# Optimization experiments

Measured on AMD Instinct MI355X. Metric: run time of the kernel, lower is better.

## Reference

```python
import jax, jax.numpy as jnp
import numpy as np

N_NODES = 100000
N_EDGES = 3200000
IN_CH, HID, OUT_CH = 128, 16, 64


def gcn_conv(x, W, b, row, col, n_nodes):
    # PyG GCNConv: add self loops, symmetric deg^{-1/2} normalization,
    # linear transform, scatter-add aggregation at target nodes (col).
    x = x @ W  # [N, out]
    deg = jax.ops.segment_sum(jnp.ones_like(col, dtype=x.dtype), col,
                              num_segments=n_nodes)  # includes self loops
    inv_sqrt = jnp.where(deg > 0, jax.lax.rsqrt(deg), 0.0)
    norm = inv_sqrt[row] * inv_sqrt[col]  # [E+N]
    msgs = x[row] * norm[:, None]  # gather + scale
    out = jax.ops.segment_sum(msgs, col, num_segments=n_nodes)
    return out + b


def setup_inputs() -> dict:
    key = jax.random.key(0)
    ks = jax.random.split(key, 12)
    x = jax.random.normal(ks[0], (N_NODES, IN_CH), dtype=jnp.float32)
    edge_index = jax.random.randint(ks[1], (2, N_EDGES), 0, N_NODES, dtype=jnp.int64)

    def glorot(k, fan_in, fan_out):
        s = jnp.sqrt(6.0 / (fan_in + fan_out))
        return jax.random.uniform(k, (fan_in, fan_out), jnp.float32, -s, s)

    return {
        'x': x,
        'edge_index': edge_index,
        'conv1_W': glorot(ks[2], IN_CH, HID),
        'conv1_b': jnp.zeros((HID,), jnp.float32),
        'conv2_W': glorot(ks[3], HID, OUT_CH),
        'conv2_b': jnp.zeros((OUT_CH,), jnp.float32),
        't1_W': glorot(ks[4], IN_CH, HID),
        't1_b': jnp.zeros((HID,), jnp.float32),
        't2_W': glorot(ks[5], HID, OUT_CH),
        't2_b': jnp.zeros((OUT_CH,), jnp.float32),
    }


def reference(x, edge_index, conv1_W, conv1_b, conv2_W, conv2_b,
              t1_W, t1_b, t2_W, t2_b):
    n = x.shape[0]
    # add self loops once (fixed shape)
    loops = jnp.arange(n, dtype=edge_index.dtype)
    row = jnp.concatenate([edge_index[0], loops])
    col = jnp.concatenate([edge_index[1], loops])

    identity1 = x @ t1_W + t1_b
    h = jax.nn.relu(gcn_conv(x, conv1_W, conv1_b, row, col, n)) + identity1
    identity2 = h @ t2_W + t2_b
    out = jax.nn.relu(gcn_conv(h, conv2_W, conv2_b, row, col, n)) + identity2
    return out
```

## Files before the change

### kernel.cpp

```cpp
#include <hip/hip_runtime.h>

#define INCH 128
#define C1   16
#define C2   64
#define LOCB 7
#define BNODES (1 << LOCB)
#define CAP  8192
#define ROWBITS 17
#define ROWMASK ((1 << ROWBITS) - 1)
#define SENT 0xFFFFFFFFu
#define ACC2P 9
#define FXS   16384.0f
#define INVFX 6.103515625e-05f
#define FXBH  524288.5f
#define BSH   19
#define BKT_T 1024
#define AGG_T 512

typedef int iv4 __attribute__((ext_vector_type(4)));
typedef unsigned long long ulv2 __attribute__((ext_vector_type(2)));

__global__ void binit_kernel(int* __restrict__ gcur, int K) {
    int t = blockIdx.x * blockDim.x + threadIdx.x;
    if (t < K) gcur[t] = t * CAP;
}

__global__ __launch_bounds__(BKT_T) void bucket_kernel(
    const int* __restrict__ row, const int* __restrict__ col,
    int* __restrict__ gcur, int* __restrict__ barr,
    int e, int n, int K, int nblocks)
{
    __shared__ int cnt[1024];
    __shared__ int cur[1024];
    __shared__ int sst[1024];
    int tid = threadIdx.x;
    int e4 = e >> 2;
    long b0 = (long)blockIdx.x * e4 / nblocks;
    long b1 = (long)(blockIdx.x + 1) * e4 / nblocks;
    const iv4* c4p = (const iv4*)col;
    const iv4* r4p = (const iv4*)row;
    cnt[tid] = 0;
    __syncthreads();
    for (long i = b0 + tid; i < b1; i += BKT_T) {
        iv4 c4 = c4p[i], r4 = r4p[i];
        #pragma unroll
        for (int k = 0; k < 4; ++k) {
            unsigned c = (unsigned)c4[k], r = (unsigned)r4[k];
            if (c < (unsigned)n && r < (unsigned)n)
                atomicAdd(&cnt[c >> LOCB], 1);
        }
    }
    if (blockIdx.x == 0) {
        for (int i = e4 * 4 + tid; i < e; i += BKT_T) {
            unsigned c = (unsigned)col[i], r = (unsigned)row[i];
            if (c < (unsigned)n && r < (unsigned)n)
                atomicAdd(&cnt[c >> LOCB], 1);
        }
    }
    __syncthreads();
    if (tid < K) {
        int c = cnt[tid];
        int start = c ? atomicAdd(&gcur[tid], (c + 15) & ~15) : 0;
        cur[tid] = start;
        sst[tid] = start;
    }
    __syncthreads();
    for (long i = b0 + tid; i < b1; i += BKT_T) {
        iv4 c4 = c4p[i], r4 = r4p[i];
        #pragma unroll
        for (int k = 0; k < 4; ++k) {
            unsigned c = (unsigned)c4[k], r = (unsigned)r4[k];
            if (c < (unsigned)n && r < (unsigned)n) {
                int b = c >> LOCB;
                int slot = atomicAdd(&cur[b], 1);
                if ((unsigned)slot < (unsigned)((b + 1) * CAP))
                    barr[slot] = (int)(r | ((c & (BNODES - 1)) << ROWBITS));
            }
        }
    }
    if (blockIdx.x == 0) {
        for (int i = e4 * 4 + tid; i < e; i += BKT_T) {
            unsigned c = (unsigned)col[i], r = (unsigned)row[i];
            if (c < (unsigned)n && r < (unsigned)n) {
                int b = c >> LOCB;
                int slot = atomicAdd(&cur[b], 1);
                if ((unsigned)slot < (unsigned)((b + 1) * CAP))
                    barr[slot] = (int)(r | ((c & (BNODES - 1)) << ROWBITS));
            }
        }
    }
    __syncthreads();
    if (tid < K) {
        int c = cnt[tid];
        if (c) {
            int start = sst[tid];
            int end = start + c;
            int re  = start + ((c + 15) & ~15);
            int lim = (tid + 1) * CAP;
            if (end > lim) end = lim;
            if (re  > lim) re  = lim;
            for (int j = end; j < re; ++j) barr[j] = (int)SENT;
        }
    }
}

__global__ __launch_bounds__(AGG_T) void degree_kernel(
    const int* __restrict__ barr, const int* __restrict__ gcur,
    int* __restrict__ deg, int n)
{
    __shared__ int lcnt[BNODES];
    int b = blockIdx.x, tid = threadIdx.x;
    if (tid < BNODES) lcnt[tid] = 0;
    __syncthreads();
    int base = b * CAP;
    int len = gcur[b] - base;
    if (len < 0) len = 0;
    if (len > CAP) len = CAP;
    int len4 = len >> 2;
    const iv4* b4 = (const iv4*)(barr + base);
    for (int i = tid; i < len4; i += AGG_T) {
        iv4 p4 = b4[i];
        #pragma unroll
        for (int k = 0; k < 4; ++k) {
            unsigned pk = (unsigned)p4[k];
            if ((pk & ROWMASK) < (unsigned)n)
                atomicAdd(&lcnt[(pk >> ROWBITS) & (BNODES - 1)], 1);
        }
    }
    __syncthreads();
    if (tid < BNODES) {
        int node = (b << LOCB) + tid;
        if (node < n) deg[node] = lcnt[tid];
    }
}

__global__ __launch_bounds__(256) void linear1_kernel(
    const float* __restrict__ x, const float* __restrict__ W1,
    const float* __restrict__ T1, const float* __restrict__ t1b,
    const int* __restrict__ deg,
    unsigned* __restrict__ xW1u, float* __restrict__ xT1, int n)
{
    __shared__ float Wc[INCH][32];
    __shared__ float xs[16][INCH + 4];
    int tid = threadIdx.x;

    for (int i = tid; i < INCH * C1; i += 256) {
        int k = i / C1, c = i % C1;
        Wc[k][c]      = W1[i];
        Wc[k][c + 16] = T1[i];
    }
    int node0 = blockIdx.x * 16;
    for (int i = tid; i < 16 * (INCH / 4); i += 256) {
        int r = i / (INCH / 4);
        int cc = i % (INCH / 4);
        int node = node0 + r;
        float4 v = make_float4(0.f, 0.f, 0.f, 0.f);
        if (node < n) v = ((const float4*)x)[(size_t)node * (INCH / 4) + cc];
        ((float4*)&xs[r][0])[cc] = v;
    }
    __syncthreads();

    int ch = tid & 15, nl = tid >> 4;
    int node = node0 + nl;
    if (node >= n) return;
    float a1 = 0.f, a2 = 0.f;
    #pragma unroll
    for (int k = 0; k < INCH; ++k) {
        float xv = xs[nl][k];
        a1 += xv * Wc[k][ch];
        a2 += xv * Wc[k][ch + 16];
    }
    float ic = rsqrtf((float)(deg[node] + 1));
    xW1u[(node << 4) + ch] = (unsigned)(a1 * ic * FXS + FXBH);
    xT1[(node << 4) + ch]  = a2 + t1b[ch];
}

#define EDGE_GS(PK, GA, GB)                                                   \
    do {                                                                      \
        if (((PK) & ROWMASK) < un) {                                          \
            unsigned long long* _a = &acc[(((PK) >> ROWBITS) & (BNODES - 1))][tb]; \
            atomicAdd(&_a[0], (GA)[0]);                                       \
            atomicAdd(&_a[1], (GA)[1]);                                       \
            atomicAdd(&_a[2], (GB)[0]);                                       \
            atomicAdd(&_a[3], (GB)[1]);                                       \
        }                                                                     \
    } while (0)

#define GATHER_SCATTER(SRCBUF)                                                \
    {                                                                         \
        int jj = tid >> 1;                                                    \
        for (int i0 = jj * 4; i0 + 3 < len; i0 += (AGG_T * 2)) {              \
            iv4 w = *(const iv4*)(bp + i0);                                   \
            unsigned s0 = (unsigned)w[0] & ROWMASK, s1 = (unsigned)w[1] & ROWMASK; \
            unsigned s2 = (unsigned)w[2] & ROWMASK, s3 = (unsigned)w[3] & ROWMASK; \
            unsigned c0 = s0 < un ? s0 : 0u, c1 = s1 < un ? s1 : 0u;          \
            unsigned c2 = s2 < un ? s2 : 0u, c3 = s3 < un ? s3 : 0u;          \
            const ulv2* p0 = (const ulv2*)(SRCBUF + ((size_t)c0 << 4) + chb); \
            const ulv2* p1 = (const ulv2*)(SRCBUF + ((size_t)c1 << 4) + chb); \
            const ulv2* p2 = (const ulv2*)(SRCBUF + ((size_t)c2 << 4) + chb); \
            const ulv2* p3 = (const ulv2*)(SRCBUF + ((size_t)c3 << 4) + chb); \
            ulv2 ga0 = p0[0], gb0 = p0[1];                                    \
            ulv2 ga1 = p1[0], gb1 = p1[1];                                    \
            ulv2 ga2 = p2[0], gb2 = p2[1];                                    \
            ulv2 ga3 = p3[0], gb3 = p3[1];                                    \
            EDGE_GS((unsigned)w[0], ga0, gb0);                                \
            EDGE_GS((unsigned)w[1], ga1, gb1);                                \
            EDGE_GS((unsigned)w[2], ga2, gb2);                                \
            EDGE_GS((unsigned)w[3], ga3, gb3);                                \
        }                                                                     \
    }

__global__ __launch_bounds__(AGG_T) void agg1_bucket_kernel(
    const int* __restrict__ barr, const int* __restrict__ gcur,
    const int* __restrict__ deg, const unsigned* __restrict__ xW1u,
    const float* __restrict__ xT1, const float* __restrict__ b1,
    float* __restrict__ h, unsigned* __restrict__ hu, int n)
{
    __shared__ unsigned long long acc[BNODES][ACC2P];
    int b = blockIdx.x, tid = threadIdx.x;
    for (int i = tid; i < BNODES * ACC2P; i += AGG_T) (&acc[0][0])[i] = 0ull;
    __syncthreads();

    int base = b * CAP;
    int len = gcur[b] - base;
    if (len < 0) len = 0;
    if (len > CAP) len = CAP;
    const int* bp = barr + base;
    unsigned un = (unsigned)n;
    int chb = (tid & 1) << 3;
    int tb  = (tid & 1) << 2;

    GATHER_SCATTER(xW1u)
    __syncthreads();

    const unsigned* au = (const unsigned*)&acc[0][0];
    for (int t = tid; t < BNODES * C1; t += AGG_T) {
        int loc = t >> 4, ch = t & 15;
        int node = (b << LOCB) + loc;
        if (node >= n) continue;
        int idx = (node << 4) + ch;
        int dg = deg[node];
        unsigned wd = au[loc * (2 * ACC2P) + ch];
        int tot = (int)(wd + xW1u[idx] - ((unsigned)(dg + 1) << BSH));
        float ic = rsqrtf((float)(dg + 1));
        float v = (float)tot * INVFX * ic + b1[ch];
        float hv = fmaxf(v, 0.f) + xT1[idx];
        h[idx]  = hv;
        hu[idx] = (unsigned)(hv * ic * FXS + FXBH);
    }
}

__global__ __launch_bounds__(AGG_T) void agg2_bucket_kernel(
    const int* __restrict__ barr, const int* __restrict__ gcur,
    const int* __restrict__ deg, const unsigned* __restrict__ hu,
    const float* __restrict__ h,
    const float* __restrict__ W2, const float* __restrict__ T2,
    const float* __restrict__ b2, const float* __restrict__ t2b,
    float* __restrict__ out, int n)
{
    __shared__ unsigned long long acc[BNODES][ACC2P];
    __shared__ float Wc[C1][128];
    __shared__ float h_s[BNODES][C1];
    __shared__ float accf[BNODES][C1 + 1];
    int b = blockIdx.x, tid = threadIdx.x;
    for (int i = tid; i < BNODES * ACC2P; i += AGG_T) (&acc[0][0])[i] = 0ull;
    for (int i = tid; i < C1 * 128; i += AGG_T) {
        int k = i >> 7, c = i & 127;
        Wc[k][c] = (c < 64) ? W2[k * C2 + c] : T2[k * C2 + (c - 64)];
    }
    {
        int node0 = b << LOCB;
        for (int t = tid; t < BNODES * C1 / 4; t += AGG_T) {
            float4 v = make_float4(0.f, 0.f, 0.f, 0.f);
            if (node0 + (t >> 2) < n) v = ((const float4*)h)[(size_t)node0 * 4 + t];
            ((float4*)&h_s[0][0])[t] = v;
        }
    }
    __syncthreads();

    int base = b * CAP;
    int len = gcur[b] - base;
    if (len < 0) len = 0;
    if (len > CAP) len = CAP;
    const int* bp = barr + base;
    unsigned un = (unsigned)n;
    int chb = (tid & 1) << 3;
    int tb  = (tid & 1) << 2;

    GATHER_SCATTER(hu)
    __syncthreads();

    const unsigned* au = (const unsigned*)&acc[0][0];
    for (int t = tid; t < BNODES * C1; t += AGG_T) {
        int loc = t >> 4, ch = t & 15;
        int node = (b << LOCB) + loc;
        float v = 0.f;
        if (node < n) {
            int dg = deg[node];
            unsigned wd = au[loc * (2 * ACC2P) + ch];
            int tot = (int)(wd + hu[(node << 4) + ch] - ((unsigned)(dg + 1) << BSH));
            v = (float)tot * INVFX * rsqrtf((float)(dg + 1));
        }
        accf[loc][ch] = v;
    }
    __syncthreads();

    int och = tid & 63, g = tid >> 6;
    float w1r[C1], w2r[C1];
    #pragma unroll
    for (int k = 0; k < C1; ++k) { w1r[k] = Wc[k][och]; w2r[k] = Wc[k][och + 64]; }
    float bb = b2[och], tb2 = t2b[och];
    for (int q = 0; q < 16; ++q) {
        int loc = (g << 4) + q;
        int node2 = (b << LOCB) + loc;
        if (node2 >= n) continue;
        float s1 = bb, s2 = tb2;
        #pragma unroll
        for (int k = 0; k < C1; ++k) {
            s1 += accf[loc][k] * w1r[k];
            s2 += h_s[loc][k]  * w2r[k];
        }
        out[(size_t)node2 * C2 + och] = fmaxf(s1, 0.f) + s2;
    }
}

extern "C" void kernel_launch(void* const* d_in, const int* in_sizes, int n_in,
                              void* d_out, int out_size, void* d_ws, size_t ws_size,
                              hipStream_t stream) {
    const float* x   = (const float*)d_in[0];
    const int*   ei  = (const int*)d_in[1];
    const float* W1  = (const float*)d_in[2];
    const float* b1  = (const float*)d_in[3];
    const float* W2  = (const float*)d_in[4];
    const float* b2  = (const float*)d_in[5];
    const float* T1  = (const float*)d_in[6];
    const float* t1b = (const float*)d_in[7];
    const float* T2  = (const float*)d_in[8];
    const float* t2b = (const float*)d_in[9];
    float* out = (float*)d_out;

    const int n = in_sizes[0] / INCH;
    const int e = in_sizes[1] / 2;
    const int* row = ei;
    const int* col = ei + e;
    const int K = (n + BNODES - 1) >> LOCB;

    char* ws = (char*)d_ws;
    int*      gcur = (int*)ws;                        ws += 4096;
    int*      deg  = (int*)ws;                        ws += (size_t)n * 4;
    float*    xT1  = (float*)ws;                      ws += (size_t)n * C1 * 4;
    float*    h    = (float*)ws;                      ws += (size_t)n * C1 * 4;
    unsigned* xW1u = (unsigned*)ws;                   ws += (size_t)n * C1 * 4;
    unsigned* hu   = (unsigned*)ws;                   ws += (size_t)n * C1 * 4;
    int*      barr = (int*)ws;                        ws += (size_t)K * CAP * 4;

    const int nbb = 390;

    binit_kernel  <<<(K + 255) / 256, 256, 0, stream>>>(gcur, K);
    bucket_kernel <<<nbb, BKT_T, 0, stream>>>(row, col, gcur, barr, e, n, K, nbb);
    degree_kernel <<<K, AGG_T, 0, stream>>>(barr, gcur, deg, n);

    linear1_kernel <<<(n + 15) / 16, 256, 0, stream>>>(x, W1, T1, t1b, deg, xW1u, xT1, n);
    agg1_bucket_kernel<<<K, AGG_T, 0, stream>>>(barr, gcur, deg, xW1u, xT1, b1, h, hu, n);
    agg2_bucket_kernel<<<K, AGG_T, 0, stream>>>(barr, gcur, deg, hu, h,
                                                W2, T2, b2, t2b, out, n);
}
```

Baseline: 268.9 us.

## Compress gathered node features to 16-bit fixed point with clamping

```diff
diff --git a/kernel.cpp b/kernel.cpp
--- a/kernel.cpp
+++ b/kernel.cpp
@@ -10,15 +10,14 @@
 #define ROWMASK ((1 << ROWBITS) - 1)
 #define SENT 0xFFFFFFFFu
 #define ACC2P 9
-#define FXS   16384.0f
-#define INVFX 6.103515625e-05f
-#define FXBH  524288.5f
-#define BSH   19
+#define FXS   512.0f
+#define INVFX 0.001953125f
+#define U16B  32768.5f
+#define BSH   15
 #define BKT_T 1024
 #define AGG_T 512
 
 typedef int iv4 __attribute__((ext_vector_type(4)));
-typedef unsigned long long ulv2 __attribute__((ext_vector_type(2)));
 
 __global__ void binit_kernel(int* __restrict__ gcur, int K) {
     int t = blockIdx.x * blockDim.x + threadIdx.x;
@@ -134,11 +133,16 @@
     }
 }
 
+__device__ __forceinline__ unsigned short enc16(float v) {
+    float c = fminf(fmaxf(v, -63.0f), 63.0f);
+    return (unsigned short)(c * FXS + U16B);
+}
+
 __global__ __launch_bounds__(256) void linear1_kernel(
     const float* __restrict__ x, const float* __restrict__ W1,
     const float* __restrict__ T1, const float* __restrict__ t1b,
     const int* __restrict__ deg,
-    unsigned* __restrict__ xW1u, float* __restrict__ xT1, int n)
+    unsigned short* __restrict__ xu16, float* __restrict__ xT1, int n)
 {
     __shared__ float Wc[INCH][32];
     __shared__ float xs[16][INCH + 4];
@@ -171,22 +175,24 @@
         a2 += xv * Wc[k][ch + 16];
     }
     float ic = rsqrtf((float)(deg[node] + 1));
-    xW1u[(node << 4) + ch] = (unsigned)(a1 * ic * FXS + FXBH);
+    xu16[(node << 4) + ch] = enc16(a1 * ic);
     xT1[(node << 4) + ch]  = a2 + t1b[ch];
 }
 
-#define EDGE_GS(PK, GA, GB)                                                   \
+#define EDGE_GS(PK, G)                                                        \
     do {                                                                      \
         if (((PK) & ROWMASK) < un) {                                          \
             unsigned long long* _a = &acc[(((PK) >> ROWBITS) & (BNODES - 1))][tb]; \
-            atomicAdd(&_a[0], (GA)[0]);                                       \
-            atomicAdd(&_a[1], (GA)[1]);                                       \
-            atomicAdd(&_a[2], (GB)[0]);                                       \
-            atomicAdd(&_a[3], (GB)[1]);                                       \
+            _Pragma("unroll")                                                 \
+            for (int _j = 0; _j < 4; ++_j) {                                  \
+                unsigned _d = (unsigned)(G)[_j];                              \
+                atomicAdd(&_a[_j],                                            \
+                    ((unsigned long long)(_d >> 16) << 32) | (_d & 0xFFFFu)); \
+            }                                                                 \
         }                                                                     \
     } while (0)
 
-#define GATHER_SCATTER(SRCBUF)                                                \
+#define GATHER_SCATTER(TBL)                                                   \
     {                                                                         \
         int jj = tid >> 1;                                                    \
         for (int i0 = jj * 4; i0 + 3 < len; i0 += (AGG_T * 2)) {              \
@@ -195,26 +201,22 @@
             unsigned s2 = (unsigned)w[2] & ROWMASK, s3 = (unsigned)w[3] & ROWMASK; \
             unsigned c0 = s0 < un ? s0 : 0u, c1 = s1 < un ? s1 : 0u;          \
             unsigned c2 = s2 < un ? s2 : 0u, c3 = s3 < un ? s3 : 0u;          \
-            const ulv2* p0 = (const ulv2*)(SRCBUF + ((size_t)c0 << 4) + chb); \
-            const ulv2* p1 = (const ulv2*)(SRCBUF + ((size_t)c1 << 4) + chb); \
-            const ulv2* p2 = (const ulv2*)(SRCBUF + ((size_t)c2 << 4) + chb); \
-            const ulv2* p3 = (const ulv2*)(SRCBUF + ((size_t)c3 << 4) + chb); \
-            ulv2 ga0 = p0[0], gb0 = p0[1];                                    \
-            ulv2 ga1 = p1[0], gb1 = p1[1];                                    \
-            ulv2 ga2 = p2[0], gb2 = p2[1];                                    \
-            ulv2 ga3 = p3[0], gb3 = p3[1];                                    \
-            EDGE_GS((unsigned)w[0], ga0, gb0);                                \
-            EDGE_GS((unsigned)w[1], ga1, gb1);                                \
-            EDGE_GS((unsigned)w[2], ga2, gb2);                                \
-            EDGE_GS((unsigned)w[3], ga3, gb3);                                \
+            iv4 g0 = *(const iv4*)(TBL + ((size_t)c0 << 3) + tb4);            \
+            iv4 g1 = *(const iv4*)(TBL + ((size_t)c1 << 3) + tb4);            \
+            iv4 g2 = *(const iv4*)(TBL + ((size_t)c2 << 3) + tb4);            \
+            iv4 g3 = *(const iv4*)(TBL + ((size_t)c3 << 3) + tb4);            \
+            EDGE_GS((unsigned)w[0], g0);                                      \
+            EDGE_GS((unsigned)w[1], g1);                                      \
+            EDGE_GS((unsigned)w[2], g2);                                      \
+            EDGE_GS((unsigned)w[3], g3);                                      \
         }                                                                     \
     }
 
 __global__ __launch_bounds__(AGG_T) void agg1_bucket_kernel(
     const int* __restrict__ barr, const int* __restrict__ gcur,
-    const int* __restrict__ deg, const unsigned* __restrict__ xW1u,
+    const int* __restrict__ deg, const unsigned short* __restrict__ xu16,
     const float* __restrict__ xT1, const float* __restrict__ b1,
-    float* __restrict__ h, unsigned* __restrict__ hu, int n)
+    float* __restrict__ h, unsigned short* __restrict__ hu16, int n)
 {
     __shared__ unsigned long long acc[BNODES][ACC2P];
     int b = blockIdx.x, tid = threadIdx.x;
@@ -226,11 +228,12 @@
     if (len < 0) len = 0;
     if (len > CAP) len = CAP;
     const int* bp = barr + base;
+    const unsigned* tblw = (const unsigned*)xu16;
     unsigned un = (unsigned)n;
-    int chb = (tid & 1) << 3;
+    int tb4 = (tid & 1) << 2;
     int tb  = (tid & 1) << 2;
 
-    GATHER_SCATTER(xW1u)
+    GATHER_SCATTER(tblw)
     __syncthreads();
 
     const unsigned* au = (const unsigned*)&acc[0][0];
@@ -241,18 +244,18 @@
         int idx = (node << 4) + ch;
         int dg = deg[node];
         unsigned wd = au[loc * (2 * ACC2P) + ch];
-        int tot = (int)(wd + xW1u[idx] - ((unsigned)(dg + 1) << BSH));
+        int tot = (int)(wd + xu16[idx] - ((unsigned)(dg + 1) << BSH));
         float ic = rsqrtf((float)(dg + 1));
         float v = (float)tot * INVFX * ic + b1[ch];
         float hv = fmaxf(v, 0.f) + xT1[idx];
-        h[idx]  = hv;
-        hu[idx] = (unsigned)(hv * ic * FXS + FXBH);
+        h[idx]    = hv;
+        hu16[idx] = enc16(hv * ic);
     }
 }
 
 __global__ __launch_bounds__(AGG_T) void agg2_bucket_kernel(
     const int* __restrict__ barr, const int* __restrict__ gcur,
-    const int* __restrict__ deg, const unsigned* __restrict__ hu,
+    const int* __restrict__ deg, const unsigned short* __restrict__ hu16,
     const float* __restrict__ h,
     const float* __restrict__ W2, const float* __restrict__ T2,
     const float* __restrict__ b2, const float* __restrict__ t2b,
@@ -283,11 +286,12 @@
     if (len < 0) len = 0;
     if (len > CAP) len = CAP;
     const int* bp = barr + base;
+    const unsigned* tblw = (const unsigned*)hu16;
     unsigned un = (unsigned)n;
-    int chb = (tid & 1) << 3;
+    int tb4 = (tid & 1) << 2;
     int tb  = (tid & 1) << 2;
 
-    GATHER_SCATTER(hu)
+    GATHER_SCATTER(tblw)
     __syncthreads();
 
     const unsigned* au = (const unsigned*)&acc[0][0];
@@ -298,7 +302,7 @@
         if (node < n) {
             int dg = deg[node];
             unsigned wd = au[loc * (2 * ACC2P) + ch];
-            int tot = (int)(wd + hu[(node << 4) + ch] - ((unsigned)(dg + 1) << BSH));
+            int tot = (int)(wd + hu16[(node << 4) + ch] - ((unsigned)(dg + 1) << BSH));
             v = (float)tot * INVFX * rsqrtf((float)(dg + 1));
         }
         accf[loc][ch] = v;
@@ -346,13 +350,13 @@
     const int K = (n + BNODES - 1) >> LOCB;
 
     char* ws = (char*)d_ws;
-    int*      gcur = (int*)ws;                        ws += 4096;
-    int*      deg  = (int*)ws;                        ws += (size_t)n * 4;
-    float*    xT1  = (float*)ws;                      ws += (size_t)n * C1 * 4;
-    float*    h    = (float*)ws;                      ws += (size_t)n * C1 * 4;
-    unsigned* xW1u = (unsigned*)ws;                   ws += (size_t)n * C1 * 4;
-    unsigned* hu   = (unsigned*)ws;                   ws += (size_t)n * C1 * 4;
-    int*      barr = (int*)ws;                        ws += (size_t)K * CAP * 4;
+    int*            gcur = (int*)ws;                  ws += 4096;
+    int*            deg  = (int*)ws;                  ws += (size_t)n * 4;
+    float*          xT1  = (float*)ws;                ws += (size_t)n * C1 * 4;
+    float*          h    = (float*)ws;                ws += (size_t)n * C1 * 4;
+    unsigned short* xu16 = (unsigned short*)ws;       ws += (size_t)n * C1 * 2;
+    unsigned short* hu16 = (unsigned short*)ws;       ws += (size_t)n * C1 * 2;
+    int*            barr = (int*)ws;                  ws += (size_t)K * CAP * 4;
 
     const int nbb = 390;
 
@@ -360,8 +364,8 @@
     bucket_kernel <<<nbb, BKT_T, 0, stream>>>(row, col, gcur, barr, e, n, K, nbb);
     degree_kernel <<<K, AGG_T, 0, stream>>>(barr, gcur, deg, n);
 
-    linear1_kernel <<<(n + 15) / 16, 256, 0, stream>>>(x, W1, T1, t1b, deg, xW1u, xT1, n);
-    agg1_bucket_kernel<<<K, AGG_T, 0, stream>>>(barr, gcur, deg, xW1u, xT1, b1, h, hu, n);
-    agg2_bucket_kernel<<<K, AGG_T, 0, stream>>>(barr, gcur, deg, hu, h,
+    linear1_kernel <<<(n + 15) / 16, 256, 0, stream>>>(x, W1, T1, t1b, deg, xu16, xT1, n);
+    agg1_bucket_kernel<<<K, AGG_T, 0, stream>>>(barr, gcur, deg, xu16, xT1, b1, h, hu16, n);
+    agg2_bucket_kernel<<<K, AGG_T, 0, stream>>>(barr, gcur, deg, hu16, h,
                                                 W2, T2, b2, t2b, out, n);
 }
```

New measurement: 250.9 us. 6.7% less time.
